# Kernel optimization log

Measured on AMD Instinct MI355X. Metric: run time of the kernel, lower is better.

The kernel has to match this reference:

```python
import jax, jax.numpy as jnp
import numpy as np
from jax import lax

K = 20
ALPHA = 0.1
N_NODES = 100000
N_EDGES = 3200000


def setup_inputs() -> dict:
    key = jax.random.key(0)
    k1, k2, k3, k4, k5, k6 = jax.random.split(key, 6)
    x = jax.random.normal(k1, (N_NODES, 512), dtype=jnp.float32)
    edge_index = jax.random.randint(k2, (2, N_EDGES), 0, N_NODES, dtype=jnp.int32)
    W1 = jax.random.normal(k3, (512, 128), dtype=jnp.float32) * 0.05
    b1 = jax.random.normal(k4, (128,), dtype=jnp.float32) * 0.05
    W2 = jax.random.normal(k5, (128, 40), dtype=jnp.float32) * 0.05
    b2 = jax.random.normal(k6, (40,), dtype=jnp.float32) * 0.05
    return {"x": x, "edge_index": edge_index, "W1": W1, "b1": b1, "W2": W2, "b2": b2}


def reference(x, edge_index, W1, b1, W2, b2):
    N = x.shape[0]
    # MLP encoder (dropout is identity in eval mode)
    h = jax.nn.relu(x @ W1 + b1)          # [N, 128]
    h = jax.nn.relu(h @ W2 + b2)          # [N, num_classes]

    # gcn_norm with self-loops (PyG APPNP default: normalize=True, add_self_loops=True)
    loop = jnp.arange(N, dtype=edge_index.dtype)
    row = jnp.concatenate([edge_index[0], loop])  # source nodes
    col = jnp.concatenate([edge_index[1], loop])  # target nodes
    deg = jax.ops.segment_sum(jnp.ones_like(col, dtype=h.dtype), col, num_segments=N)
    dinv = jnp.where(deg > 0, lax.rsqrt(deg), 0.0)
    norm = dinv[row] * dinv[col]          # [E + N]

    h0 = h

    def step(z, _):
        msg = norm[:, None] * z[row]                       # gather + scale
        agg = jax.ops.segment_sum(msg, col, num_segments=N)  # scatter-add
        z = (1.0 - ALPHA) * agg + ALPHA * h0
        return z, None

    z, _ = lax.scan(step, h0, None, length=K)
    return z
```

## Files before the change

kernel.cpp:

```cpp
#include <hip/hip_runtime.h>
#include <hip/hip_bf16.h>

#define K_ITERS 20
#define F_IN 512
#define F_HID 128
#define F_OUT 40
#define PWAVES 8192


typedef const float __attribute__((address_space(1)))* glb_fp;
typedef float __attribute__((address_space(3)))* lds_fp;

__global__ void k_hist(const int* __restrict__ col, int E, int* __restrict__ cnt){
  int e = blockIdx.x*blockDim.x + threadIdx.x;
  if (e < E) atomicAdd(&cnt[col[e]], 1);
}

__global__ void k_dinv(const int* __restrict__ cnt, int N, float* __restrict__ dinv){
  int i = blockIdx.x*blockDim.x + threadIdx.x;
  if (i < N) dinv[i] = rsqrtf((float)(cnt[i] + 1));
}

__device__ __forceinline__ int pad6(int c){ return ((c + 5)/6)*6; }

__global__ void k_scan1(const int* __restrict__ cnt, int N, int* __restrict__ bsum){
  __shared__ int sd[256];
  int base = blockIdx.x*2048 + threadIdx.x*8;
  int t = threadIdx.x;
  int s = 0;
  #pragma unroll
  for (int j=0;j<8;++j){ int i=base+j; if (i<N) s += pad6(cnt[i]+1); }
  sd[t] = s; __syncthreads();
  for (int off=1; off<256; off<<=1){
    int v = (t>=off)? sd[t-off] : 0;
    __syncthreads();
    sd[t] += v;
    __syncthreads();
  }
  if (t==255) bsum[blockIdx.x] = sd[255];
}
__global__ void k_scan2(const int* __restrict__ bsum, int NB, int* __restrict__ boff,
                        int* __restrict__ rp, int N){
  __shared__ int sd[256];
  int t = threadIdx.x;
  int v = (t < NB) ? bsum[t] : 0;
  sd[t] = v; __syncthreads();
  for (int off=1; off<256; off<<=1){
    int u = (t>=off)? sd[t-off] : 0;
    __syncthreads();
    sd[t] += u;
    __syncthreads();
  }
  if (t < NB) boff[t] = sd[t] - v;
  if (t == NB-1) rp[N] = sd[t];
}
__global__ void k_scan3(const int* __restrict__ cnt, int N, const int* __restrict__ boff,
                        int* __restrict__ rp){
  __shared__ int sd[256];
  int base = blockIdx.x*2048 + threadIdx.x*8;
  int t = threadIdx.x;
  int c[8]; int s = 0;
  #pragma unroll
  for (int j=0;j<8;++j){ int i=base+j; c[j] = (i<N)? pad6(cnt[i]+1) : 0; s += c[j]; }
  sd[t] = s; __syncthreads();
  for (int off=1; off<256; off<<=1){
    int v = (t>=off)? sd[t-off] : 0;
    __syncthreads();
    sd[t] += v;
    __syncthreads();
  }
  int run = sd[t] - s + boff[blockIdx.x];
  #pragma unroll
  for (int j=0;j<8;++j){ int i=base+j; if (i<N) rp[i] = run; run += c[j]; }
}

__global__ void k_scatter(const int* __restrict__ row, const int* __restrict__ col, int E,
                          const int* __restrict__ rp, int* __restrict__ cur,
                          const float* __restrict__ dinv, int2* __restrict__ pair){
  int e = blockIdx.x*blockDim.x + threadIdx.x;
  if (e >= E) return;
  int r = row[e], c = col[e];
  int p = rp[c] + atomicAdd(&cur[c], 1);
  pair[p] = make_int2(r, __float_as_int(dinv[r]*dinv[c]));
}
__global__ void k_selfpair(int N, const int* __restrict__ rp, int* __restrict__ cur,
                           const float* __restrict__ dinv, int2* __restrict__ pair){
  int n = blockIdx.x*blockDim.x + threadIdx.x;
  if (n >= N) return;
  int p = rp[n] + atomicAdd(&cur[n], 1);
  float di = dinv[n];
  pair[p] = make_int2(n, __float_as_int(di*di));
}

__global__ __launch_bounds__(256) void k_mlp(const float* __restrict__ x,
                      const float* __restrict__ W1, const float* __restrict__ b1,
                      const float* __restrict__ W2, const float* __restrict__ b2,
                      float* __restrict__ h0, int N){
  __shared__ float lds[12288];
  const int t    = threadIdx.x;
  const int th   = t & 31;
  const int tn   = t >> 5;
  const int lane = t & 63;
  const int wv   = __builtin_amdgcn_readfirstlane(t >> 6);
  const int nb   = blockIdx.x * 64;

  auto stage_w = [&](int kt, int b){
    const float* gs = W1 + kt*(32*128) + wv*1024 + lane*4;
    int lo = __builtin_amdgcn_readfirstlane((b*4096 + wv*1024) * 4);
    #pragma unroll
    for (int i=0;i<4;++i){
      __builtin_amdgcn_global_load_lds((glb_fp)(gs + i*256),
        (lds_fp)((char*)lds + lo + i*1024), 16, 0, 0);
    }
  };
  auto stage_x = [&](int kt, int b){
    #pragma unroll
    for (int s=0;s<2;++s){
      int i = wv*2 + s;
      int flat = i*256 + lane*4;
      int n = flat >> 5;
      int kk = flat & 31;
      int node = nb + n; if (node >= N) node = N-1;
      const float* gs = x + (size_t)node*F_IN + kt*32 + kk;
      int lo = __builtin_amdgcn_readfirstlane(32768 + b*8192 + i*1024);
      __builtin_amdgcn_global_load_lds((glb_fp)gs,
        (lds_fp)((char*)lds + lo), 16, 0, 0);
    }
  };

  float acc[8][4];
  {
    float4 bb = *(const float4*)(b1 + th*4);
    #pragma unroll
    for (int j=0;j<8;++j){ acc[j][0]=bb.x; acc[j][1]=bb.y; acc[j][2]=bb.z; acc[j][3]=bb.w; }
  }

  stage_w(0, 0); stage_x(0, 0);
  __syncthreads();

  for (int kt=0; kt<16; ++kt){
    const int cur = kt & 1;
    if (kt < 15){ stage_w(kt+1, cur^1); stage_x(kt+1, cur^1); }
    const float* xb = lds + 8192 + cur*2048;
    const float* wb = lds + cur*4096;
    #pragma unroll
    for (int c=0;c<8;++c){
      float4 xv[8];
      #pragma unroll
      for (int j=0;j<8;++j) xv[j] = *(const float4*)(xb + (tn*8+j)*32 + c*4);
      const float* wl = wb + c*512 + th*4;
      float4 wa = *(const float4*)(wl);
      float4 wb4 = *(const float4*)(wl + 128);
      float4 wc = *(const float4*)(wl + 256);
      float4 wd = *(const float4*)(wl + 384);
      #pragma unroll
      for (int j=0;j<8;++j){
        acc[j][0] += xv[j].x*wa.x; acc[j][1] += xv[j].x*wa.y; acc[j][2] += xv[j].x*wa.z; acc[j][3] += xv[j].x*wa.w;
        acc[j][0] += xv[j].y*wb4.x; acc[j][1] += xv[j].y*wb4.y; acc[j][2] += xv[j].y*wb4.z; acc[j][3] += xv[j].y*wb4.w;
        acc[j][0] += xv[j].z*wc.x; acc[j][1] += xv[j].z*wc.y; acc[j][2] += xv[j].z*wc.z; acc[j][3] += xv[j].z*wc.w;
        acc[j][0] += xv[j].w*wd.x; acc[j][1] += xv[j].w*wd.y; acc[j][2] += xv[j].w*wd.z; acc[j][3] += xv[j].w*wd.w;
      }
    }
    __syncthreads();
  }

  #pragma unroll
  for (int h=0; h<4; ++h){
    const int hid = th*4 + h;
    float4 v0 = make_float4(fmaxf(acc[0][h],0.f), fmaxf(acc[1][h],0.f),
                            fmaxf(acc[2][h],0.f), fmaxf(acc[3][h],0.f));
    float4 v1 = make_float4(fmaxf(acc[4][h],0.f), fmaxf(acc[5][h],0.f),
                            fmaxf(acc[6][h],0.f), fmaxf(acc[7][h],0.f));
    *(float4*)&lds[hid*68 + tn*8]     = v0;
    *(float4*)&lds[hid*68 + tn*8 + 4] = v1;
  }
  __syncthreads();

  const int c0 = wv*10;
  float a2[10];
  #pragma unroll
  for (int i=0;i<10;++i) a2[i] = b2[c0+i];
  #pragma unroll 4
  for (int k=0;k<F_HID;++k){
    const float hv = lds[k*68 + lane];
    #pragma unroll
    for (int i=0;i<10;++i) a2[i] += hv * W2[k*F_OUT + c0 + i];
  }
  const int gn = nb + lane;
  if (gn < N){
    float* o = h0 + (size_t)gn*F_OUT + c0;
    #pragma unroll
    for (int i=0;i<10;++i) o[i] = fmaxf(a2[i], 0.f);
  }
}

__global__ __launch_bounds__(256, 8) void k_prop(const int* __restrict__ rp,
                      const int2* __restrict__ pair, const float* __restrict__ zin,
                      const float* __restrict__ h0, float* __restrict__ zout,
                      int N, int npw){
  __shared__ float red[4][6][40];
  const int wv   = __builtin_amdgcn_readfirstlane((int)(threadIdx.x >> 6));
  const int W    = blockIdx.x*4 + wv;
  const int lane = threadIdx.x & 63;
  int e_lane = lane/10; if (e_lane > 5) e_lane = 5;
  int qd = lane - e_lane*10; if (qd > 9) qd = 9;
  const int qoff = qd*4;

  for (int k=0; k<npw; ++k){
    const int n = W + k*PWAVES;
    if (n >= N) break;
    const int beg = rp[n];
    const int nch = (rp[n+1] - beg)/6;

    float ax=0.f, ay=0.f, az=0.f, aw=0.f;
    const int2* mp = pair + beg + e_lane;

    int2 mA = mp[0];
    float4 zA = *(const float4*)(zin + (size_t)mA.x*F_OUT + qoff);
    int c = 0;
    while (true){
      int2 mB; float4 zB;
      const bool hb = (c+1 < nch);
      if (hb){
        mB = mp[(c+1)*6];
        zB = *(const float4*)(zin + (size_t)mB.x*F_OUT + qoff);
      }
      const float nm = __int_as_float(mA.y);
      ax += nm*zA.x; ay += nm*zA.y; az += nm*zA.z; aw += nm*zA.w;
      if (++c >= nch) break;
      mA = mB; zA = zB;
    }

    if (lane < 60) *(float4*)&red[wv][e_lane][qoff] = make_float4(ax,ay,az,aw);
    if (lane < F_OUT){
      float s = red[wv][0][lane] + red[wv][1][lane] + red[wv][2][lane]
              + red[wv][3][lane] + red[wv][4][lane] + red[wv][5][lane];
      const size_t idx = (size_t)n*F_OUT + lane;
      zout[idx] = 0.9f*s + 0.1f*h0[idx];
    }
  }
}

extern "C" void kernel_launch(void* const* d_in, const int* in_sizes, int n_in,
                              void* d_out, int out_size, void* d_ws, size_t ws_size,
                              hipStream_t stream){
  const float* x  = (const float*)d_in[0];
  const int*   ei = (const int*)d_in[1];
  const float* W1 = (const float*)d_in[2];
  const float* b1 = (const float*)d_in[3];
  const float* W2 = (const float*)d_in[4];
  const float* b2 = (const float*)d_in[5];
  int N = in_sizes[0] / F_IN;
  int E = in_sizes[1] / 2;
  const int* row = ei;
  const int* col = ei + E;
  size_t EP = (size_t)E + 7ull*(size_t)N;

  char* w = (char*)d_ws;
  auto alloc = [&](size_t bytes)->void*{ void* p = w; w += (bytes + 255) & ~255ull; return p; };
  int*   cnt      = (int*)  alloc((size_t)N*4);
  int*   cur      = (int*)  alloc((size_t)N*4);
  int*   rp       = (int*)  alloc(((size_t)N+1)*4);
  float* dinv     = (float*)alloc((size_t)N*4);
  int NB = (N + 2047)/2048;
  int*   bsum     = (int*)  alloc((size_t)NB*4);
  int*   boff     = (int*)  alloc((size_t)NB*4);
  int2*  pair     = (int2*) alloc(EP*8);
  float* h0       = (float*)alloc((size_t)N*F_OUT*4);
  float* zA       = (float*)alloc((size_t)N*F_OUT*4);
  float* zB       = (float*)alloc((size_t)N*F_OUT*4);

  (void)hipMemsetAsync(cnt, 0, (size_t)N*4, stream);
  (void)hipMemsetAsync(cur, 0, (size_t)N*4, stream);
  (void)hipMemsetAsync(pair, 0, EP*8, stream);

  int ge = (E + 255)/256;
  k_hist    <<<ge, 256, 0, stream>>>(col, E, cnt);
  k_dinv    <<<(N+255)/256, 256, 0, stream>>>(cnt, N, dinv);
  k_scan1   <<<NB, 256, 0, stream>>>(cnt, N, bsum);
  k_scan2   <<<1, 256, 0, stream>>>(bsum, NB, boff, rp, N);
  k_scan3   <<<NB, 256, 0, stream>>>(cnt, N, boff, rp);
  k_scatter <<<ge, 256, 0, stream>>>(row, col, E, rp, cur, dinv, pair);
  k_selfpair<<<(N+255)/256, 256, 0, stream>>>(N, rp, cur, dinv, pair);

  k_mlp<<<(N+63)/64, 256, 0, stream>>>(x, W1, b1, W2, b2, h0, N);

  int npw = (N + PWAVES - 1)/PWAVES;
  float* zi = h0; float* zo = zA;
  for (int it=0; it<K_ITERS; ++it){
    float* dst = (it == K_ITERS-1) ? (float*)d_out : zo;
    k_prop<<<PWAVES/4, 256, 0, stream>>>(rp, pair, zi, h0, dst, N, npw);
    float* nxt = (it==0) ? zB : zi;
    zi = zo; zo = nxt;
  }
}
```

Before: 2.790 ms.

## Split features into 8-wide slabs and propagate one slab per wave

Node features are stored as five slabs of 8 floats per node, and the propagation kernel launches one wave per (slab, node). Each lane gathers a single float from the slab, neighbor lists are padded to multiples of 8, and the partial sums are reduced with shuffles instead of LDS. The intent is to keep each slab's working set (N*8 floats) cache-resident and to drop the LDS reduction. In exchange, the edge pair list is read five times per iteration, each gather is a 32-byte segment, and the grid becomes very large.

```diff
diff --git a/kernel.cpp b/kernel.cpp
--- a/kernel.cpp
+++ b/kernel.cpp
@@ -5,7 +5,7 @@
 #define F_IN 512
 #define F_HID 128
 #define F_OUT 40
-#define PWAVES 8192
+#define NSLAB 5
 
 
 typedef const float __attribute__((address_space(1)))* glb_fp;
@@ -21,7 +21,7 @@
   if (i < N) dinv[i] = rsqrtf((float)(cnt[i] + 1));
 }
 
-__device__ __forceinline__ int pad6(int c){ return ((c + 5)/6)*6; }
+__device__ __forceinline__ int pad8(int c){ return (c + 8) & ~7; }
 
 __global__ void k_scan1(const int* __restrict__ cnt, int N, int* __restrict__ bsum){
   __shared__ int sd[256];
@@ -29,7 +29,7 @@
   int t = threadIdx.x;
   int s = 0;
   #pragma unroll
-  for (int j=0;j<8;++j){ int i=base+j; if (i<N) s += pad6(cnt[i]+1); }
+  for (int j=0;j<8;++j){ int i=base+j; if (i<N) s += pad8(cnt[i]); }
   sd[t] = s; __syncthreads();
   for (int off=1; off<256; off<<=1){
     int v = (t>=off)? sd[t-off] : 0;
@@ -61,7 +61,7 @@
   int t = threadIdx.x;
   int c[8]; int s = 0;
   #pragma unroll
-  for (int j=0;j<8;++j){ int i=base+j; c[j] = (i<N)? pad6(cnt[i]+1) : 0; s += c[j]; }
+  for (int j=0;j<8;++j){ int i=base+j; c[j] = (i<N)? pad8(cnt[i]) : 0; s += c[j]; }
   sd[t] = s; __syncthreads();
   for (int off=1; off<256; off<<=1){
     int v = (t>=off)? sd[t-off] : 0;
@@ -95,7 +95,7 @@
 __global__ __launch_bounds__(256) void k_mlp(const float* __restrict__ x,
                       const float* __restrict__ W1, const float* __restrict__ b1,
                       const float* __restrict__ W2, const float* __restrict__ b2,
-                      float* __restrict__ h0, int N){
+                      float* __restrict__ h0s, int N){
   __shared__ float lds[12288];
   const int t    = threadIdx.x;
   const int th   = t & 31;
@@ -188,56 +188,52 @@
   }
   const int gn = nb + lane;
   if (gn < N){
-    float* o = h0 + (size_t)gn*F_OUT + c0;
-    #pragma unroll
-    for (int i=0;i<10;++i) o[i] = fmaxf(a2[i], 0.f);
-  }
-}
-
-__global__ __launch_bounds__(256, 8) void k_prop(const int* __restrict__ rp,
-                      const int2* __restrict__ pair, const float* __restrict__ zin,
-                      const float* __restrict__ h0, float* __restrict__ zout,
-                      int N, int npw){
-  __shared__ float red[4][6][40];
+    #pragma unroll
+    for (int i=0;i<10;++i){
+      int c = c0 + i;
+      h0s[((size_t)(c>>3)*N + gn)*8 + (c&7)] = fmaxf(a2[i], 0.f);
+    }
+  }
+}
+
+__global__ __launch_bounds__(256) void k_prop(const int* __restrict__ rp,
+                      const int2* __restrict__ pair,
+                      const float* __restrict__ zin, const float* __restrict__ h0s,
+                      float* __restrict__ zout, float* __restrict__ dout,
+                      int N, int BPS, int last){
   const int wv   = __builtin_amdgcn_readfirstlane((int)(threadIdx.x >> 6));
-  const int W    = blockIdx.x*4 + wv;
+  const int bid  = blockIdx.x;
+  const int slab = bid / BPS;
+  const int node = (bid - slab*BPS)*4 + wv;
   const int lane = threadIdx.x & 63;
-  int e_lane = lane/10; if (e_lane > 5) e_lane = 5;
-  int qd = lane - e_lane*10; if (qd > 9) qd = 9;
-  const int qoff = qd*4;
-
-  for (int k=0; k<npw; ++k){
-    const int n = W + k*PWAVES;
-    if (n >= N) break;
-    const int beg = rp[n];
-    const int nch = (rp[n+1] - beg)/6;
-
-    float ax=0.f, ay=0.f, az=0.f, aw=0.f;
-    const int2* mp = pair + beg + e_lane;
-
-    int2 mA = mp[0];
-    float4 zA = *(const float4*)(zin + (size_t)mA.x*F_OUT + qoff);
-    int c = 0;
-    while (true){
-      int2 mB; float4 zB;
-      const bool hb = (c+1 < nch);
-      if (hb){
-        mB = mp[(c+1)*6];
-        zB = *(const float4*)(zin + (size_t)mB.x*F_OUT + qoff);
-      }
-      const float nm = __int_as_float(mA.y);
-      ax += nm*zA.x; ay += nm*zA.y; az += nm*zA.z; aw += nm*zA.w;
-      if (++c >= nch) break;
-      mA = mB; zA = zB;
-    }
-
-    if (lane < 60) *(float4*)&red[wv][e_lane][qoff] = make_float4(ax,ay,az,aw);
-    if (lane < F_OUT){
-      float s = red[wv][0][lane] + red[wv][1][lane] + red[wv][2][lane]
-              + red[wv][3][lane] + red[wv][4][lane] + red[wv][5][lane];
-      const size_t idx = (size_t)n*F_OUT + lane;
-      zout[idx] = 0.9f*s + 0.1f*h0[idx];
-    }
+  const int e8   = lane >> 3;
+  const int f    = lane & 7;
+  if (node >= N) return;
+
+  const int beg = rp[node];
+  const int nch = (rp[node+1] - beg) >> 3;
+  const float* zs = zin + (size_t)slab*N*8;
+
+  float acc = 0.f;
+  int2 m = pair[beg + e8];
+  for (int c=0; c<nch; ++c){
+    const int pn = (c+1 < nch) ? (c+1) : c;
+    int2 mn = pair[beg + pn*8 + e8];
+    const float nm = __int_as_float(m.y);
+    const float zv = zs[(size_t)m.x*8 + f];
+    acc += nm * zv;
+    m = mn;
+  }
+
+  acc += __shfl_xor(acc, 8);
+  acc += __shfl_xor(acc, 16);
+  acc += __shfl_xor(acc, 32);
+
+  if (lane < 8){
+    const size_t hi = ((size_t)slab*N + node)*8 + f;
+    const float v = 0.9f*acc + 0.1f*h0s[hi];
+    if (last) dout[(size_t)node*F_OUT + slab*8 + f] = v;
+    else      zout[hi] = v;
   }
 }
 
@@ -254,7 +250,7 @@
   int E = in_sizes[1] / 2;
   const int* row = ei;
   const int* col = ei + E;
-  size_t EP = (size_t)E + 7ull*(size_t)N;
+  size_t EP = (size_t)E + 8ull*(size_t)N;
 
   char* w = (char*)d_ws;
   auto alloc = [&](size_t bytes)->void*{ void* p = w; w += (bytes + 255) & ~255ull; return p; };
@@ -266,7 +262,7 @@
   int*   bsum     = (int*)  alloc((size_t)NB*4);
   int*   boff     = (int*)  alloc((size_t)NB*4);
   int2*  pair     = (int2*) alloc(EP*8);
-  float* h0       = (float*)alloc((size_t)N*F_OUT*4);
+  float* h0s      = (float*)alloc((size_t)N*F_OUT*4);
   float* zA       = (float*)alloc((size_t)N*F_OUT*4);
   float* zB       = (float*)alloc((size_t)N*F_OUT*4);
 
@@ -283,13 +279,14 @@
   k_scatter <<<ge, 256, 0, stream>>>(row, col, E, rp, cur, dinv, pair);
   k_selfpair<<<(N+255)/256, 256, 0, stream>>>(N, rp, cur, dinv, pair);
 
-  k_mlp<<<(N+63)/64, 256, 0, stream>>>(x, W1, b1, W2, b2, h0, N);
-
-  int npw = (N + PWAVES - 1)/PWAVES;
-  float* zi = h0; float* zo = zA;
+  k_mlp<<<(N+63)/64, 256, 0, stream>>>(x, W1, b1, W2, b2, h0s, N);
+
+  int BPS = (N + 3)/4;
+  int grid = BPS * NSLAB;
+  float* zi = h0s; float* zo = zA;
   for (int it=0; it<K_ITERS; ++it){
-    float* dst = (it == K_ITERS-1) ? (float*)d_out : zo;
-    k_prop<<<PWAVES/4, 256, 0, stream>>>(rp, pair, zi, h0, dst, N, npw);
+    int last = (it == K_ITERS-1) ? 1 : 0;
+    k_prop<<<grid, 256, 0, stream>>>(rp, pair, zi, h0s, zo, (float*)d_out, N, BPS, last);
     float* nxt = (it==0) ? zB : zi;
     zi = zo; zo = nxt;
   }
```

Result: slower. 5.635 ms (+102.0%).
